# Kernel optimization log

Hardware: AMD Instinct MI355X
Metric: run time of the kernel (lower is better)

Reference implementation:

```python
import jax, jax.numpy as jnp
import numpy as np

N_EMBD = 1024
N_HEAD = 16
HEAD = N_EMBD // N_HEAD


def setup_inputs() -> dict:
    key = jax.random.key(0)
    ks = jax.random.split(key, 5)
    B, T = 2, 2048
    s = 1.0 / np.sqrt(N_EMBD)
    return {
        "x": jax.random.normal(ks[0], (B, T, N_EMBD), dtype=jnp.float32),
        "w_attn": jax.random.normal(ks[1], (N_EMBD, 3 * N_EMBD), dtype=jnp.float32) * s,
        "b_attn": jnp.zeros((3 * N_EMBD,), dtype=jnp.float32),
        "w_proj": jax.random.normal(ks[2], (N_EMBD, N_EMBD), dtype=jnp.float32) * s,
        "b_proj": jnp.zeros((N_EMBD,), dtype=jnp.float32),
    }


def reference(x, w_attn, b_attn, w_proj, b_proj):
    B, T, C = x.shape
    qkv = x @ w_attn + b_attn                      # [B,T,3C]
    q, k, v = jnp.split(qkv, 3, axis=-1)
    def heads(t):
        return t.reshape(B, T, N_HEAD, HEAD).transpose(0, 2, 1, 3)  # [B,H,T,D]
    q, k, v = heads(q), heads(k), heads(v)
    scale = 1.0 / np.sqrt(HEAD).astype(np.float32)
    scores = jnp.einsum('bhqd,bhkd->bhqk', q, k) * scale
    causal = jnp.tril(jnp.ones((T, T), dtype=bool))
    scores = jnp.where(causal, scores, -jnp.inf)
    attn = jax.nn.softmax(scores, axis=-1)
    out = jnp.einsum('bhqk,bhkd->bhqd', attn, v)   # [B,H,T,D]
    out = out.transpose(0, 2, 1, 3).reshape(B, T, C)
    return out @ w_proj + b_proj
```

## Files before the change

### kernel.cpp

```cpp
#include <hip/hip_runtime.h>
#include <stdint.h>

#define N_EMBD 1024
#define N_HEADv 16
#define HEADv 64
#define Bv 2
#define Tv 2048
#define BT (Bv*Tv)
#define C3 (3*N_EMBD)

typedef __attribute__((ext_vector_type(8))) short bf16x8;
typedef __attribute__((ext_vector_type(4))) float f32x4;

typedef __attribute__((address_space(3))) uint32_t lds_u32;
typedef const __attribute__((address_space(1))) uint32_t glb_u32;

__device__ __forceinline__ void gload_lds16(const void* g, void* l){
  __builtin_amdgcn_global_load_lds((glb_u32*)g, (lds_u32*)l, 16, 0, 0);
}

__device__ __forceinline__ unsigned short f2bf(float f){
  union { float f; uint32_t u; } v; v.f = f;
  uint32_t u = v.u;
  uint32_t r = u + 0x7FFFu + ((u>>16)&1u);
  return (unsigned short)(r>>16);
}
__device__ __forceinline__ uint32_t f2bf_fast(float f){
  union { float f; uint32_t u; } v; v.f = f;
  return (v.u + 0x8000u) >> 16;
}
__device__ __forceinline__ float bf2f(unsigned short s){
  union { uint32_t u; float f; } v; v.u = ((uint32_t)s)<<16; return v.f;
}

__global__ void k_cvt_bf16(const float* __restrict__ in, unsigned short* __restrict__ out, long n){
  long i = ((long)blockIdx.x*blockDim.x + threadIdx.x)*8;
  if(i >= n) return;
  float4 a = *reinterpret_cast<const float4*>(in+i);
  float4 b = *reinterpret_cast<const float4*>(in+i+4);
  union { int4 v; unsigned short s[8]; } o;
  o.s[0]=f2bf(a.x); o.s[1]=f2bf(a.y); o.s[2]=f2bf(a.z); o.s[3]=f2bf(a.w);
  o.s[4]=f2bf(b.x); o.s[5]=f2bf(b.y); o.s[6]=f2bf(b.z); o.s[7]=f2bf(b.w);
  *reinterpret_cast<int4*>(out+i) = o.v;
}

__global__ void k_transpose_bf16(const float* __restrict__ in, unsigned short* __restrict__ out, int K, int N){
  __shared__ float tile[64][65];
  int n0 = blockIdx.x*64, k0 = blockIdx.y*64;
  int t = threadIdx.x;
  #pragma unroll
  for(int p=0;p<4;p++){
    int row = (t>>4) + p*16;
    int col4 = (t&15)*4;
    float4 v = *reinterpret_cast<const float4*>(&in[(size_t)(k0+row)*N + n0 + col4]);
    tile[row][col4+0]=v.x; tile[row][col4+1]=v.y; tile[row][col4+2]=v.z; tile[row][col4+3]=v.w;
  }
  __syncthreads();
  #pragma unroll
  for(int p=0;p<4;p++){
    int nrow = (t>>4) + p*16;
    int kc = (t&15)*4;
    ushort4 o;
    o.x = f2bf(tile[kc+0][nrow]);
    o.y = f2bf(tile[kc+1][nrow]);
    o.z = f2bf(tile[kc+2][nrow]);
    o.w = f2bf(tile[kc+3][nrow]);
    *reinterpret_cast<ushort4*>(&out[(size_t)(n0+nrow)*K + k0 + kc]) = o;
  }
}

template<int MODE>
__global__ __launch_bounds__(256) void k_gemm(
    const unsigned short* __restrict__ A,
    const unsigned short* __restrict__ Bt,
    const float* __restrict__ bias,
    void* __restrict__ Cout,
    int M, int N, int K)
{
  const int BK=64;
  __shared__ unsigned short As[128*BK];
  __shared__ unsigned short Bs[128*BK];
  int m0 = blockIdx.y*128, n0 = blockIdx.x*128;
  int t = threadIdx.x, lane = t&63, wid = t>>6;
  int wm = (wid>>1)*64, wn = (wid&1)*64;
  int g = lane>>4, r16 = lane&15;
  int rl  = lane>>3;
  int cle = (((lane&7) ^ rl) * 8);
  int rsw = r16 & 7;
  f32x4 acc[4][4] = {};

  for(int k0=0;k0<K;k0+=BK){
    __syncthreads();
    #pragma unroll
    for(int c=0;c<4;c++){
      int rb = wid*32 + c*8;
      gload_lds16(&A [(size_t)(m0+rb+rl)*K + k0 + cle], &As[rb*BK]);
      gload_lds16(&Bt[(size_t)(n0+rb+rl)*K + k0 + cle], &Bs[rb*BK]);
    }
    __syncthreads();
    bf16x8 af[2][4], bfr[2][4];
    #pragma unroll
    for(int ks=0;ks<2;ks++){
      #pragma unroll
      for(int mi=0;mi<4;mi++)
        af[ks][mi]  = *reinterpret_cast<const bf16x8*>(&As[(wm+mi*16+r16)*BK + (((ks*4+g)^rsw)*8)]);
      #pragma unroll
      for(int ni=0;ni<4;ni++)
        bfr[ks][ni] = *reinterpret_cast<const bf16x8*>(&Bs[(wn+ni*16+r16)*BK + (((ks*4+g)^rsw)*8)]);
    }
    #pragma unroll
    for(int ks=0;ks<2;ks++)
      #pragma unroll
      for(int mi=0;mi<4;mi++)
        #pragma unroll
        for(int ni=0;ni<4;ni++){
          if(MODE==0)
            acc[mi][ni] = __builtin_amdgcn_mfma_f32_16x16x32_bf16(af[ks][mi], bfr[ks][ni], acc[mi][ni], 0,0,0);
          else
            acc[mi][ni] = __builtin_amdgcn_mfma_f32_16x16x32_bf16(bfr[ks][ni], af[ks][mi], acc[mi][ni], 0,0,0);
        }
  }

  if(MODE==0){
    int which = (n0+wn)>>10;
    int h = ((n0+wn)&1023)>>6;
    int bb = m0>>11;
    int tt0 = (m0&2047) + wm;
    unsigned short* base = (unsigned short*)Cout;
    if(which < 2){
      unsigned short* dst = base + (size_t)which*BT*N_EMBD
                          + (((size_t)bb*N_HEADv + h)*Tv + tt0)*HEADv;
      #pragma unroll
      for(int ni=0;ni<4;ni++){
        float bv = bias[n0+wn+ni*16+r16];
        int d = ni*16 + r16;
        #pragma unroll
        for(int mi=0;mi<4;mi++)
          #pragma unroll
          for(int reg=0;reg<4;reg++){
            int tt = mi*16 + g*4 + reg;
            dst[(size_t)tt*HEADv + d] = f2bf(acc[mi][ni][reg] + bv);
          }
      }
    } else {
      unsigned short* dst = base + 2ll*BT*N_EMBD
                          + (((size_t)bb*N_HEADv + h)*HEADv)*Tv + tt0;
      #pragma unroll
      for(int ni=0;ni<4;ni++){
        float bv = bias[n0+wn+ni*16+r16];
        int d = ni*16 + r16;
        #pragma unroll
        for(int mi=0;mi<4;mi++)
          #pragma unroll
          for(int reg=0;reg<4;reg++){
            int tt = mi*16 + g*4 + reg;
            dst[(size_t)d*Tv + tt] = f2bf(acc[mi][ni][reg] + bv);
          }
      }
    }
  } else {
    float* out = (float*)Cout;
    #pragma unroll
    for(int mi=0;mi<4;mi++){
      int m = m0+wm+mi*16+r16;
      #pragma unroll
      for(int ni=0;ni<4;ni++){
        int n = n0+wn+ni*16+g*4;
        float4 b4 = *reinterpret_cast<const float4*>(&bias[n]);
        float4 o4;
        o4.x = acc[mi][ni][0] + b4.x;
        o4.y = acc[mi][ni][1] + b4.y;
        o4.z = acc[mi][ni][2] + b4.z;
        o4.w = acc[mi][ni][3] + b4.w;
        *reinterpret_cast<float4*>(&out[(size_t)m*N + n]) = o4;
      }
    }
  }
}

__global__ __launch_bounds__(256) void k_attn(
    const unsigned short* __restrict__ QKV,
    unsigned short* __restrict__ O,
    unsigned short* __restrict__ partO,
    float2* __restrict__ stats)
{
  __shared__ unsigned short Ks[2][64][64];
  __shared__ unsigned short Vs[2][64][64];
  __shared__ unsigned short Ps[4][16][64];
  int blk = blockIdx.x;
  int bh = blk & 31;
  int j  = blk >> 5;
  int qt, kt0, ktN; bool single;
  if(j < 16)      { qt = 16+j;  kt0 = 0;  ktN = 16;    single = false; }
  else if(j < 32) { qt = 47-j;  kt0 = 16; ktN = qt+1;  single = false; }
  else            { qt = 47-j;  kt0 = 0;  ktN = qt+1;  single = true;  }

  int t = threadIdx.x, lane=t&63, wid=t>>6;
  int g = lane>>4, r16 = lane&15;
  const unsigned short* Qp  = QKV + (size_t)bh*Tv*HEADv;
  const unsigned short* Kp  = QKV + (size_t)BT*N_EMBD + (size_t)bh*Tv*HEADv;
  const unsigned short* Vtp = QKV + 2ll*BT*N_EMBD + (size_t)bh*HEADv*Tv;
  int q0 = qt*64 + wid*16;

  bf16x8 aq[2];
  #pragma unroll
  for(int kb=0;kb<2;kb++)
    aq[kb] = *reinterpret_cast<const bf16x8*>(&Qp[(size_t)(q0+r16)*HEADv + kb*32 + g*8]);

  f32x4 oacc[4] = {};
  float m2 = -1e30f, l = 0.f;

  int r0 = t>>3, c0 = (t&7)*8;
  int r1 = r0 + 32;
  int sw0 = c0 ^ ((r0&7)<<3);
  int sw1 = c0 ^ ((r1&7)<<3);
  int rsw = (r16&7)<<3;

  int4 kc0, kc1, vc0, vc1;
  kc0 = *reinterpret_cast<const int4*>(&Kp [(size_t)(kt0*64+r0)*HEADv + c0]);
  kc1 = *reinterpret_cast<const int4*>(&Kp [(size_t)(kt0*64+r1)*HEADv + c0]);
  vc0 = *reinterpret_cast<const int4*>(&Vtp[(size_t)r0*Tv + kt0*64 + c0]);
  vc1 = *reinterpret_cast<const int4*>(&Vtp[(size_t)r1*Tv + kt0*64 + c0]);
  *reinterpret_cast<int4*>(&Ks[0][r0][sw0]) = kc0;
  *reinterpret_cast<int4*>(&Ks[0][r1][sw1]) = kc1;
  *reinterpret_cast<int4*>(&Vs[0][r0][sw0]) = vc0;
  *reinterpret_cast<int4*>(&Vs[0][r1][sw1]) = vc1;
  if(ktN - kt0 > 1){
    kc0 = *reinterpret_cast<const int4*>(&Kp [(size_t)((kt0+1)*64+r0)*HEADv + c0]);
    kc1 = *reinterpret_cast<const int4*>(&Kp [(size_t)((kt0+1)*64+r1)*HEADv + c0]);
    vc0 = *reinterpret_cast<const int4*>(&Vtp[(size_t)r0*Tv + (kt0+1)*64 + c0]);
    vc1 = *reinterpret_cast<const int4*>(&Vtp[(size_t)r1*Tv + (kt0+1)*64 + c0]);
  }
  __syncthreads();

  for(int kt=kt0; kt<ktN; ++kt){
    int cur = kt & 1;
    if(kt+1 < ktN){
      *reinterpret_cast<int4*>(&Ks[cur^1][r0][sw0]) = kc0;
      *reinterpret_cast<int4*>(&Ks[cur^1][r1][sw1]) = kc1;
      *reinterpret_cast<int4*>(&Vs[cur^1][r0][sw0]) = vc0;
      *reinterpret_cast<int4*>(&Vs[cur^1][r1][sw1]) = vc1;
      if(kt+2 < ktN){
        kc0 = *reinterpret_cast<const int4*>(&Kp [(size_t)((kt+2)*64+r0)*HEADv + c0]);
        kc1 = *reinterpret_cast<const int4*>(&Kp [(size_t)((kt+2)*64+r1)*HEADv + c0]);
        vc0 = *reinterpret_cast<const int4*>(&Vtp[(size_t)r0*Tv + (kt+2)*64 + c0]);
        vc1 = *reinterpret_cast<const int4*>(&Vtp[(size_t)r1*Tv + (kt+2)*64 + c0]);
      }
    }

    f32x4 sacc[4];
    __builtin_amdgcn_s_setprio(1);
    #pragma unroll
    for(int nb=0;nb<4;nb++){
      sacc[nb] = (f32x4){0.f,0.f,0.f,0.f};
      #pragma unroll
      for(int kb=0;kb<2;kb++){
        bf16x8 bk = *reinterpret_cast<const bf16x8*>(&Ks[cur][nb*16+r16][(kb*32+g*8) ^ rsw]);
        sacc[nb] = __builtin_amdgcn_mfma_f32_16x16x32_bf16(bk, aq[kb], sacc[nb],0,0,0);
      }
    }
    __builtin_amdgcn_s_setprio(0);

    const float SC = 0.18033688f;
    bool diag = (kt == qt);
    float pv[4][4];
    float mxnb[4];
    #pragma unroll
    for(int nb=0;nb<4;nb++){
      #pragma unroll
      for(int reg=0;reg<4;reg++){
        float s = sacc[nb][reg] * SC;
        if(diag){
          int keyin = nb*16 + g*4 + reg;
          if(keyin > wid*16 + r16) s = -1e30f;
        }
        pv[nb][reg] = s;
      }
      mxnb[nb] = fmaxf(fmaxf(pv[nb][0],pv[nb][1]), fmaxf(pv[nb][2],pv[nb][3]));
    }
    float mx = fmaxf(fmaxf(mxnb[0],mxnb[1]), fmaxf(mxnb[2],mxnb[3]));
    mx = fmaxf(mx, __shfl_xor(mx, 16, 64));
    mx = fmaxf(mx, __shfl_xor(mx, 32, 64));

    if(!__all(mx - m2 <= 11.5f)){
      float mn = fmaxf(m2, mx);
      float alpha = __builtin_amdgcn_exp2f(m2 - mn);
      l *= alpha;
      #pragma unroll
      for(int nb=0;nb<4;nb++)
        #pragma unroll
        for(int reg=0;reg<4;reg++) oacc[nb][reg] *= alpha;
      m2 = mn;
    }

    float rsnb[4];
    #pragma unroll
    for(int nb=0;nb<4;nb++){
      #pragma unroll
      for(int reg=0;reg<4;reg++)
        pv[nb][reg] = __builtin_amdgcn_exp2f(pv[nb][reg] - m2);
      rsnb[nb] = (pv[nb][0]+pv[nb][1]) + (pv[nb][2]+pv[nb][3]);
    }
    float rs = (rsnb[0]+rsnb[1]) + (rsnb[2]+rsnb[3]);
    rs += __shfl_xor(rs, 16, 64);
    rs += __shfl_xor(rs, 32, 64);
    l += rs;

    #pragma unroll
    for(int nb=0;nb<4;nb++){
      union { uint32_t u[2]; int2 v; } w;
      w.u[0] = f2bf_fast(pv[nb][0]) | (f2bf_fast(pv[nb][1])<<16);
      w.u[1] = f2bf_fast(pv[nb][2]) | (f2bf_fast(pv[nb][3])<<16);
      *reinterpret_cast<int2*>(&Ps[wid][r16][(nb*16+g*4) ^ rsw]) = w.v;
    }

    __builtin_amdgcn_s_setprio(1);
    #pragma unroll
    for(int kb=0;kb<2;kb++){
      bf16x8 ap = *reinterpret_cast<const bf16x8*>(&Ps[wid][r16][(kb*32+g*8) ^ rsw]);
      #pragma unroll
      for(int nb=0;nb<4;nb++){
        bf16x8 bv = *reinterpret_cast<const bf16x8*>(&Vs[cur][nb*16+r16][(kb*32+g*8) ^ rsw]);
        oacc[nb] = __builtin_amdgcn_mfma_f32_16x16x32_bf16(bv, ap, oacc[nb],0,0,0);
      }
    }
    __builtin_amdgcn_s_setprio(0);
    __syncthreads();
  }

  float rinv = 1.0f / l;
  if(single){
    int b = bh >> 4, h = bh & 15;
    size_t row = (size_t)b*Tv + q0 + r16;
    #pragma unroll
    for(int nb=0;nb<4;nb++){
      ushort4 o;
      o.x = f2bf(oacc[nb][0]*rinv);
      o.y = f2bf(oacc[nb][1]*rinv);
      o.z = f2bf(oacc[nb][2]*rinv);
      o.w = f2bf(oacc[nb][3]*rinv);
      *reinterpret_cast<ushort4*>(&O[row*N_EMBD + h*HEADv + nb*16 + g*4]) = o;
    }
  } else {
    int part = j*32 + bh;
    unsigned short* po = partO + (size_t)part*4096;
    int qloc = wid*16 + r16;
    #pragma unroll
    for(int nb=0;nb<4;nb++){
      ushort4 o;
      o.x = f2bf(oacc[nb][0]*rinv);
      o.y = f2bf(oacc[nb][1]*rinv);
      o.z = f2bf(oacc[nb][2]*rinv);
      o.w = f2bf(oacc[nb][3]*rinv);
      *reinterpret_cast<ushort4*>(&po[qloc*64 + nb*16 + g*4]) = o;
    }
    if(g==0) stats[part*64 + qloc] = make_float2(m2, l);
  }
}

__global__ __launch_bounds__(256) void k_merge(
    const unsigned short* __restrict__ partO,
    const float2* __restrict__ stats,
    unsigned short* __restrict__ O)
{
  int blk = blockIdx.x;
  int bh = blk & 31, qt = 16 + (blk >> 5);
  int p0 = (qt-16)*32 + bh;
  int p1 = (47-qt)*32 + bh;
  int t = threadIdx.x;
  int q = t >> 2, d0 = (t&3)*16;
  float2 s0 = stats[p0*64 + q];
  float2 s1 = stats[p1*64 + q];
  float m = fmaxf(s0.x, s1.x);
  float w0 = s0.y * __builtin_amdgcn_exp2f(s0.x - m);
  float w1 = s1.y * __builtin_amdgcn_exp2f(s1.x - m);
  float rinv = 1.f/(w0+w1);
  w0 *= rinv; w1 *= rinv;
  const unsigned short* a = partO + (size_t)p0*4096 + q*64 + d0;
  const unsigned short* b = partO + (size_t)p1*4096 + q*64 + d0;
  int bb = bh >> 4, h = bh & 15;
  unsigned short* o = O + ((size_t)bb*Tv + qt*64 + q)*N_EMBD + h*HEADv + d0;
  #pragma unroll
  for(int half=0; half<2; ++half){
    union { int4 v; unsigned short s[8]; } ua, ub, uo;
    ua.v = *reinterpret_cast<const int4*>(a + half*8);
    ub.v = *reinterpret_cast<const int4*>(b + half*8);
    #pragma unroll
    for(int e=0;e<8;e++)
      uo.s[e] = f2bf(bf2f(ua.s[e])*w0 + bf2f(ub.s[e])*w1);
    *reinterpret_cast<int4*>(o + half*8) = uo.v;
  }
}

extern "C" void kernel_launch(void* const* d_in, const int* in_sizes, int n_in,
                              void* d_out, int out_size, void* d_ws, size_t ws_size,
                              hipStream_t stream){
  const float* x      = (const float*)d_in[0];
  const float* w_attn = (const float*)d_in[1];
  const float* b_attn = (const float*)d_in[2];
  const float* w_proj = (const float*)d_in[3];
  const float* b_proj = (const float*)d_in[4];
  char* ws = (char*)d_ws;
  unsigned short* xb  = (unsigned short*)ws;
  unsigned short* qkv = (unsigned short*)(ws + 8ll*1024*1024);
  unsigned short* ob  = (unsigned short*)(ws + 32ll*1024*1024);
  unsigned short* wat = (unsigned short*)(ws + 40ll*1024*1024);
  unsigned short* wpt = (unsigned short*)(ws + 46ll*1024*1024);
  unsigned short* partO = xb;
  float2*        stats  = (float2*)wat;

  k_cvt_bf16<<<2048,256,0,stream>>>(x, xb, (long)BT*N_EMBD);
  k_transpose_bf16<<<dim3(C3/64, N_EMBD/64),256,0,stream>>>(w_attn, wat, N_EMBD, C3);
  k_transpose_bf16<<<dim3(N_EMBD/64, N_EMBD/64),256,0,stream>>>(w_proj, wpt, N_EMBD, N_EMBD);
  k_gemm<0><<<dim3(C3/128, BT/128),256,0,stream>>>(xb, wat, b_attn, (void*)qkv, BT, C3, N_EMBD);
  k_attn<<<dim3(48*32),256,0,stream>>>(qkv, ob, partO, stats);
  k_merge<<<dim3(512),256,0,stream>>>(partO, stats, ob);
  k_gemm<1><<<dim3(N_EMBD/128, BT/128),256,0,stream>>>(ob, wpt, b_proj, d_out, BT, N_EMBD, N_EMBD);
}
```

Measured before the change: 128.7 us.

## Double-buffer GEMM LDS tiles to overlap global loads with MFMA compute

The GEMM kernel now allocates two LDS buffers for A and B and issues the async global-to-LDS loads for the next K tile before computing on the current one. This cuts the per-iteration syncthreads pair down to one and hides global load latency behind the MFMA work. It also raises wave priority around the MFMA block. LDS use doubles, which may lower occupancy.

```diff
diff --git a/kernel.cpp b/kernel.cpp
--- a/kernel.cpp
+++ b/kernel.cpp
@@ -78,8 +78,9 @@
     int M, int N, int K)
 {
   const int BK=64;
-  __shared__ unsigned short As[128*BK];
-  __shared__ unsigned short Bs[128*BK];
+  const int TSZ=128*BK;
+  __shared__ unsigned short As[2*TSZ];
+  __shared__ unsigned short Bs[2*TSZ];
   int m0 = blockIdx.y*128, n0 = blockIdx.x*128;
   int t = threadIdx.x, lane = t&63, wid = t>>6;
   int wm = (wid>>1)*64, wn = (wid&1)*64;
@@ -89,25 +90,40 @@
   int rsw = r16 & 7;
   f32x4 acc[4][4] = {};
 
-  for(int k0=0;k0<K;k0+=BK){
-    __syncthreads();
-    #pragma unroll
-    for(int c=0;c<4;c++){
-      int rb = wid*32 + c*8;
-      gload_lds16(&A [(size_t)(m0+rb+rl)*K + k0 + cle], &As[rb*BK]);
-      gload_lds16(&Bt[(size_t)(n0+rb+rl)*K + k0 + cle], &Bs[rb*BK]);
-    }
-    __syncthreads();
+  #pragma unroll
+  for(int c=0;c<4;c++){
+    int rb = wid*32 + c*8;
+    gload_lds16(&A [(size_t)(m0+rb+rl)*K + cle], &As[rb*BK]);
+    gload_lds16(&Bt[(size_t)(n0+rb+rl)*K + cle], &Bs[rb*BK]);
+  }
+  __syncthreads();
+
+  const int NIT = K/BK;
+  for(int it=0; it<NIT; ++it){
+    int cur = it & 1;
+    if(it+1 < NIT){
+      int k0 = (it+1)*BK;
+      int nxt = (cur^1)*TSZ;
+      #pragma unroll
+      for(int c=0;c<4;c++){
+        int rb = wid*32 + c*8;
+        gload_lds16(&A [(size_t)(m0+rb+rl)*K + k0 + cle], &As[nxt + rb*BK]);
+        gload_lds16(&Bt[(size_t)(n0+rb+rl)*K + k0 + cle], &Bs[nxt + rb*BK]);
+      }
+    }
+    const unsigned short* Ab = &As[cur*TSZ];
+    const unsigned short* Bb = &Bs[cur*TSZ];
     bf16x8 af[2][4], bfr[2][4];
     #pragma unroll
     for(int ks=0;ks<2;ks++){
       #pragma unroll
       for(int mi=0;mi<4;mi++)
-        af[ks][mi]  = *reinterpret_cast<const bf16x8*>(&As[(wm+mi*16+r16)*BK + (((ks*4+g)^rsw)*8)]);
+        af[ks][mi]  = *reinterpret_cast<const bf16x8*>(&Ab[(wm+mi*16+r16)*BK + (((ks*4+g)^rsw)*8)]);
       #pragma unroll
       for(int ni=0;ni<4;ni++)
-        bfr[ks][ni] = *reinterpret_cast<const bf16x8*>(&Bs[(wn+ni*16+r16)*BK + (((ks*4+g)^rsw)*8)]);
-    }
+        bfr[ks][ni] = *reinterpret_cast<const bf16x8*>(&Bb[(wn+ni*16+r16)*BK + (((ks*4+g)^rsw)*8)]);
+    }
+    __builtin_amdgcn_s_setprio(1);
     #pragma unroll
     for(int ks=0;ks<2;ks++)
       #pragma unroll
@@ -119,6 +135,8 @@
           else
             acc[mi][ni] = __builtin_amdgcn_mfma_f32_16x16x32_bf16(bfr[ks][ni], af[ks][mi], acc[mi][ni], 0,0,0);
         }
+    __builtin_amdgcn_s_setprio(0);
+    __syncthreads();
   }
 
   if(MODE==0){
```

Result: faster. 123.0 us (-4.4%).
